# Optimization experiments

Hardware: AMD Instinct MI355X
Metric: run time of the kernel (lower is better)

Reference implementation:

```python
import jax, jax.numpy as jnp
import numpy as np

N_NODES = 100000
N_EDGES = 3200000
IN_DIM = 21
HID = 64


def gcn_conv(x, W, b, src, dst, n):
    # GCNConv: out = D^{-1/2} (A + I) D^{-1/2} (x W) + b
    h = x @ W  # [n, out]
    loop = jnp.arange(n)
    src_all = jnp.concatenate([src, loop])
    dst_all = jnp.concatenate([dst, loop])
    deg = jax.ops.segment_sum(jnp.ones(src_all.shape[0], h.dtype), dst_all,
                              num_segments=n)
    dinv = jax.lax.rsqrt(jnp.maximum(deg, 1.0))  # deg >= 1 with self-loops
    norm = dinv[src_all] * dinv[dst_all]  # [E+n]
    out = jax.ops.segment_sum(h[src_all] * norm[:, None], dst_all,
                              num_segments=n)
    return out + b


def setup_inputs() -> dict:
    key = jax.random.key(0)
    ks = jax.random.split(key, 12)
    def lin(k, fan_in, fan_out):
        bound = 1.0 / np.sqrt(fan_in)
        kw, kb = jax.random.split(k)
        W = jax.random.uniform(kw, (fan_in, fan_out), jnp.float32, -bound, bound)
        b = jax.random.uniform(kb, (fan_out,), jnp.float32, -bound, bound)
        return W, b
    x = jax.random.normal(ks[0], (N_NODES, IN_DIM), jnp.float32)
    edge_index = jax.random.randint(ks[1], (2, N_EDGES), 0, N_NODES, jnp.int64)
    W1, b1 = lin(ks[2], IN_DIM, HID)
    W2, b2 = lin(ks[3], HID, 2 * HID)
    W3, b3 = lin(ks[4], 2 * HID, HID)
    Wl1, bl1 = lin(ks[5], HID, 20)
    Wl2, bl2 = lin(ks[6], 20, 1)
    return {"x": x, "edge_index": edge_index,
            "W1": W1, "b1": b1, "W2": W2, "b2": b2, "W3": W3, "b3": b3,
            "Wl1": Wl1, "bl1": bl1, "Wl2": Wl2, "bl2": bl2}


def reference(x, edge_index, W1, b1, W2, b2, W3, b3, Wl1, bl1, Wl2, bl2):
    n = x.shape[0]
    src, dst = edge_index[0], edge_index[1]
    h = jax.nn.relu(gcn_conv(x, W1, b1, src, dst, n))
    h = jax.nn.relu(gcn_conv(h, W2, b2, src, dst, n))
    h = jax.nn.relu(gcn_conv(h, W3, b3, src, dst, n))
    h = jax.nn.relu(h @ Wl1 + bl1)
    return h @ Wl2 + bl2  # [n, 1]
```

## Files before the change

### kernel.cpp

```cpp
#include <hip/hip_runtime.h>

#define DEV static __device__ __forceinline__

typedef __attribute__((ext_vector_type(8))) short short8;
typedef __attribute__((ext_vector_type(4))) float f32x4;

DEV float bf2f(unsigned short u){ union{unsigned i; float f;} a; a.i=((unsigned)u)<<16; return a.f; }
DEV unsigned short f2bf(float f){ union{unsigned i; float f;} a; a.f=f; unsigned r=a.i+0x7fffu+((a.i>>16)&1u); return (unsigned short)(r>>16); }
DEV float2 bfu2f2(unsigned v){ union{unsigned i; float f;} lo,hi; lo.i=v<<16; hi.i=v&0xffff0000u; return make_float2(lo.f,hi.f); }

#define CB_SHIFT 9
#define CB_NODES 512
#define PK_SHIFT 23
#define PK_MASK  0x7fffffu
#define CHUNK 4096
#define P_WIN 4
#define BIN_CAP 18432

__global__ __launch_bounds__(256) void coarsehist_kernel(const int* __restrict__ dst,
    int* __restrict__ bcnt, int E, int NB){
  __shared__ int h[256];
  int t=threadIdx.x;
  h[t]=0; __syncthreads();
  int i=blockIdx.x*256+t, st=gridDim.x*256;
  for(;i<E;i+=st) atomicAdd(&h[dst[i]>>CB_SHIFT],1);
  __syncthreads();
  if(t<NB && h[t]) atomicAdd(&bcnt[t],h[t]);
}

__global__ __launch_bounds__(256) void binscan_kernel(const int* __restrict__ bcnt,
    int* __restrict__ binoffs, int* __restrict__ bincur, int NB, int E){
  __shared__ int s[256];
  int t=threadIdx.x;
  int v=(t<NB)?bcnt[t]:0;
  s[t]=v; __syncthreads();
  for(int o=1;o<256;o<<=1){
    int u=(t>=o)?s[t-o]:0;
    __syncthreads();
    if(t>=o) s[t]+=u;
    __syncthreads();
  }
  int ex=s[t]-v;
  if(t<NB){ binoffs[t]=ex; bincur[t]=ex; }
  if(t==0) binoffs[NB]=E;
}

__global__ __launch_bounds__(256) void chunkscatter_kernel(const int* __restrict__ src,
    const int* __restrict__ dst, int* __restrict__ bincur, unsigned* __restrict__ tmp,
    int E, int NB){
  __shared__ int lcnt[256];
  __shared__ int lstart[256];
  __shared__ int lbase[256];
  __shared__ unsigned pk[CHUNK];
  __shared__ int gaddr[CHUNK];
  int t=threadIdx.x;
  lcnt[t]=0; __syncthreads();
  int e0=blockIdx.x*CHUNK, e1=min(e0+CHUNK,E);
  int n=e1-e0;
  unsigned pkr[16]; int binr[16]; int rnk[16];
  #pragma unroll
  for(int q=0;q<16;q++){
    int i=e0+t+q*256;
    if(i<e1){
      int d=dst[i];
      int b=d>>CB_SHIFT;
      binr[q]=b;
      pkr[q]=(unsigned)src[i]|((unsigned)(d&(CB_NODES-1))<<PK_SHIFT);
      rnk[q]=atomicAdd(&lcnt[b],1);
    }
  }
  __syncthreads();
  int c=lcnt[t];
  lstart[t]=c; __syncthreads();
  for(int o=1;o<256;o<<=1){
    int u=(t>=o)?lstart[t-o]:0;
    __syncthreads();
    if(t>=o) lstart[t]+=u;
    __syncthreads();
  }
  int ex=lstart[t]-c;
  __syncthreads();
  lstart[t]=ex;
  lbase[t]=(t<NB&&c)?atomicAdd(&bincur[t],c):0;
  __syncthreads();
  #pragma unroll
  for(int q=0;q<16;q++){
    int i=e0+t+q*256;
    if(i<e1){
      int b=binr[q];
      int p=lstart[b]+rnk[q];
      pk[p]=pkr[q];
      gaddr[p]=lbase[b]+rnk[q];
    }
  }
  __syncthreads();
  for(int p=t;p<n;p+=256) tmp[gaddr[p]]=pk[p];
}

__global__ __launch_bounds__(512) void binsort_kernel(const unsigned* __restrict__ tmp,
    const int* __restrict__ binoffs, int* __restrict__ offs, int* __restrict__ deg,
    float* __restrict__ dinv, int* __restrict__ col, int M, int WSZ){
  __shared__ int cnt[CB_NODES*P_WIN];
  __shared__ int cur[CB_NODES*P_WIN];
  __shared__ int ssum[512];
  __shared__ int pkl[BIN_CAP];
  int b=blockIdx.x, t=threadIdx.x;
  int n0=b*CB_NODES;
  int e0=binoffs[b], e1=binoffs[b+1];
  int n=e1-e0;
  bool fit=(n<=BIN_CAP);
  cnt[4*t]=0; cnt[4*t+1]=0; cnt[4*t+2]=0; cnt[4*t+3]=0;
  __syncthreads();
  for(int i=e0+t;i<e1;i+=512){
    unsigned p=tmp[i];
    int s=(int)(p&PK_MASK);
    int w=(s>=WSZ)+(s>=2*WSZ)+(s>=3*WSZ);
    atomicAdd(&cnt[(int)(p>>PK_SHIFT)*P_WIN+w],1);
  }
  __syncthreads();
  int loc[4]; int s=0;
  #pragma unroll
  for(int q=0;q<4;q++){ loc[q]=s; s+=cnt[t*4+q]; }
  ssum[t]=s; __syncthreads();
  for(int o=1;o<512;o<<=1){
    int u=(t>=o)?ssum[t-o]:0;
    __syncthreads();
    if(t>=o) ssum[t]+=u;
    __syncthreads();
  }
  int rel=ssum[t]-s;
  #pragma unroll
  for(int q=0;q<4;q++) cur[t*4+q]=rel+loc[q];
  int nn=n0+t;
  if(nn<M){
    offs[nn]=e0+rel; deg[nn]=s; dinv[nn]=rsqrtf((float)(s+1));
  }
  __syncthreads();
  for(int i=e0+t;i<e1;i+=512){
    unsigned p=tmp[i];
    int s2=(int)(p&PK_MASK);
    int w=(s2>=WSZ)+(s2>=2*WSZ)+(s2>=3*WSZ);
    int pos=atomicAdd(&cur[(int)(p>>PK_SHIFT)*P_WIN+w],1);
    if(fit) pkl[pos]=s2;
    else col[e0+pos]=s2;
  }
  __syncthreads();
  if(fit){
    for(int i=t;i<n;i+=512) col[e0+i]=pkl[i];
  }
}

__global__ __launch_bounds__(256) void scale_kernel(const float* __restrict__ x, const float* __restrict__ dinv,
    uint2* __restrict__ xs, int M){
  int idx=blockIdx.x*256+threadIdx.x;
  if(idx>=M*8) return;
  int n=idx>>3, l=idx&7;
  float dv=dinv[n];
  const float* xr=x+(size_t)n*21;
  int c=4*l;
  float f0=(c  <21)?xr[c  ]*dv:0.f;
  float f1=(c+1<21)?xr[c+1]*dv:0.f;
  float f2v=(c+2<21)?xr[c+2]*dv:0.f;
  float f3=(c+3<21)?xr[c+3]*dv:0.f;
  uint2 v;
  v.x=(unsigned)f2bf(f0)|((unsigned)f2bf(f1)<<16);
  v.y=(unsigned)f2bf(f2v)|((unsigned)f2bf(f3)<<16);
  xs[(size_t)n*8+l]=v;
}

template<int GROUP,bool BR,bool OUTBF>
DEV void agg_body(const uint2* __restrict__ xs, const int* __restrict__ col,
    const int* __restrict__ offs, const int* __restrict__ deg, const float* __restrict__ dinv,
    const float* __restrict__ bias, void* __restrict__ out, int M){
  int gid=blockIdx.x*256+threadIdx.x;
  int node=gid/GROUP, lane=gid%GROUP;
  if(node>=M) return;
  float a0,a1,a2,a3;
  {
    uint2 v=xs[(size_t)node*GROUP+lane];
    float2 p=bfu2f2(v.x), q=bfu2f2(v.y);
    a0=p.x; a1=p.y; a2=q.x; a3=q.y;
  }
  int e0=offs[node], d=deg[node];
  int i=0;
  for(;i+8<=d;i+=8){
    int s[8]; uint2 w[8];
    #pragma unroll
    for(int q=0;q<8;q++) s[q]=col[e0+i+q];
    #pragma unroll
    for(int q=0;q<8;q++) w[q]=xs[(size_t)s[q]*GROUP+lane];
    #pragma unroll
    for(int q=0;q<8;q++){
      float2 p=bfu2f2(w[q].x); a0+=p.x; a1+=p.y;
      p=bfu2f2(w[q].y); a2+=p.x; a3+=p.y;
    }
  }
  for(;i+4<=d;i+=4){
    int s[4]; uint2 w[4];
    #pragma unroll
    for(int q=0;q<4;q++) s[q]=col[e0+i+q];
    #pragma unroll
    for(int q=0;q<4;q++) w[q]=xs[(size_t)s[q]*GROUP+lane];
    #pragma unroll
    for(int q=0;q<4;q++){
      float2 p=bfu2f2(w[q].x); a0+=p.x; a1+=p.y;
      p=bfu2f2(w[q].y); a2+=p.x; a3+=p.y;
    }
  }
  for(;i<d;i++){
    uint2 w=xs[(size_t)col[e0+i]*GROUP+lane];
    float2 p=bfu2f2(w.x); a0+=p.x; a1+=p.y;
    p=bfu2f2(w.y); a2+=p.x; a3+=p.y;
  }
  float dv=dinv[node];
  a0*=dv; a1*=dv; a2*=dv; a3*=dv;
  if constexpr(BR){
    a0=fmaxf(a0+bias[4*lane  ],0.f);
    a1=fmaxf(a1+bias[4*lane+1],0.f);
    a2=fmaxf(a2+bias[4*lane+2],0.f);
    a3=fmaxf(a3+bias[4*lane+3],0.f);
  }
  if constexpr(OUTBF){
    uint2 v;
    v.x=(unsigned)f2bf(a0)|((unsigned)f2bf(a1)<<16);
    v.y=(unsigned)f2bf(a2)|((unsigned)f2bf(a3)<<16);
    ((uint2*)out)[(size_t)node*GROUP+lane]=v;
  } else {
    ((float4*)out)[(size_t)node*GROUP+lane]=make_float4(a0,a1,a2,a3);
  }
}

__global__ __launch_bounds__(256) void agg1_kernel(const uint2* xs, const int* col, const int* offs,
    const int* deg, const float* dinv, uint2* out, int M){
  agg_body<8,false,true>(xs,col,offs,deg,dinv,nullptr,out,M);
}
__global__ __launch_bounds__(256) void agg2_kernel(const uint2* xs, const int* col, const int* offs,
    const int* deg, const float* dinv, uint2* out, int M){
  agg_body<16,false,true>(xs,col,offs,deg,dinv,nullptr,out,M);
}
__global__ __launch_bounds__(256) void agg3_kernel(const uint2* xs, const int* col, const int* offs,
    const int* deg, const float* dinv, const float* bias, float4* out, int M){
  agg_body<16,true,false>(xs,col,offs,deg,dinv,bias,out,M);
}

__global__ __launch_bounds__(256) void wprep_kernel(const float* __restrict__ W,
    unsigned short* __restrict__ Warr, int KS, int RK, int N, int KN){
  int idx=blockIdx.x*256+threadIdx.x;
  if(idx>=KN) return;
  int j=idx&7, l=(idx>>3)&63, t=idx>>9;
  int ks=t%KS, nt=t/KS;
  int k=ks*32+((l>>4)<<3)+j;
  int c=nt*16+(l&15);
  float w=(k<RK)?W[(size_t)k*N+c]:0.f;
  unsigned short hi=f2bf(w);
  unsigned short lo=f2bf(w-bf2f(hi));
  Warr[idx]=hi;
  Warr[KN+idx]=lo;
}

template<int K,int NT,bool BR,bool DV>
DEV void mfma_gemm_body(const unsigned short* __restrict__ X, const unsigned short* __restrict__ Warr,
    const float* __restrict__ bias, const float* __restrict__ dinv, unsigned short* __restrict__ Out, int M){
  constexpr int KS=K/32;
  constexpr int N=NT*16;
  constexpr int KN=K*N;
  int tid=threadIdx.x;
  int lane=tid&63, wave=tid>>6;
  int rowbase=blockIdx.x*64+wave*16;
  int r=rowbase+(lane&15);
  int rc=min(r,M-1);
  const short* Xr=(const short*)(X+(size_t)rc*K+((lane>>4)<<3));
  short8 af[KS];
  #pragma unroll
  for(int ks=0;ks<KS;ks++) af[ks]=*(const short8*)(Xr+ks*32);
  const short* wp=(const short*)Warr+lane*8;
  int colv=lane&15;
  #pragma unroll
  for(int nt=0;nt<NT;nt++){
    f32x4 acc={0.f,0.f,0.f,0.f};
    const short* wnt=wp+nt*KS*512;
    #pragma unroll
    for(int ks=0;ks<KS;ks++){
      short8 bh=*(const short8*)(wnt+ks*512);
      short8 bl=*(const short8*)(wnt+KN+ks*512);
      acc=__builtin_amdgcn_mfma_f32_16x16x32_bf16(af[ks],bh,acc,0,0,0);
      acc=__builtin_amdgcn_mfma_f32_16x16x32_bf16(af[ks],bl,acc,0,0,0);
    }
    int c=nt*16+colv;
    float bv=0.f;
    if constexpr(BR) bv=bias[c];
    #pragma unroll
    for(int reg=0;reg<4;reg++){
      int row=rowbase+((lane>>4)<<2)+reg;
      if(row<M){
        float v=acc[reg];
        if constexpr(BR) v=fmaxf(v+bv,0.f);
        if constexpr(DV) v*=dinv[row];
        Out[(size_t)row*N+c]=f2bf(v);
      }
    }
  }
}

__global__ __launch_bounds__(256) void gemm1m_kernel(const unsigned short* X, const unsigned short* Warr,
    const float* bias, const float* dinv, unsigned short* Out, int M){
  mfma_gemm_body<32,4,true,true>(X,Warr,bias,dinv,Out,M);
}
__global__ __launch_bounds__(256) void gemm2m_kernel(const unsigned short* X, const unsigned short* Warr,
    const float* bias, unsigned short* Out, int M){
  mfma_gemm_body<64,8,true,false>(X,Warr,bias,nullptr,Out,M);
}
__global__ __launch_bounds__(256) void gemm3m_kernel(const unsigned short* X, const unsigned short* Warr,
    const float* dinv, unsigned short* Out, int M){
  mfma_gemm_body<128,4,false,true>(X,Warr,nullptr,dinv,Out,M);
}

__global__ __launch_bounds__(256) void mlp_kernel(const float* __restrict__ h, const float* __restrict__ W1,
    const float* __restrict__ b1, const float* __restrict__ W2, const float* __restrict__ b2,
    float* __restrict__ out, int M){
  __shared__ float W1s[64*20];
  __shared__ float b1s[20];
  __shared__ float W2s[20];
  __shared__ float b2s;
  int tid=threadIdx.x;
  for(int i=tid;i<1280;i+=256) W1s[i]=W1[i];
  if(tid<20){ b1s[tid]=b1[tid]; W2s[tid]=W2[tid]; }
  if(tid==0) b2s=b2[0];
  __syncthreads();
  int n=blockIdx.x*256+tid;
  if(n>=M) return;
  float acc[20];
  #pragma unroll
  for(int j=0;j<20;j++) acc[j]=b1s[j];
  const float4* hp=(const float4*)(h+(size_t)n*64);
  for(int k4=0;k4<16;k4++){
    float4 hv=hp[k4];
    #pragma unroll
    for(int j=0;j<20;j++){
      acc[j]=fmaf(hv.x,W1s[(k4*4+0)*20+j],acc[j]);
      acc[j]=fmaf(hv.y,W1s[(k4*4+1)*20+j],acc[j]);
      acc[j]=fmaf(hv.z,W1s[(k4*4+2)*20+j],acc[j]);
      acc[j]=fmaf(hv.w,W1s[(k4*4+3)*20+j],acc[j]);
    }
  }
  float r=b2s;
  #pragma unroll
  for(int j=0;j<20;j++) r+=fmaxf(acc[j],0.f)*W2s[j];
  out[n]=r;
}

extern "C" void kernel_launch(void* const* d_in, const int* in_sizes, int n_in,
                              void* d_out, int out_size, void* d_ws, size_t ws_size,
                              hipStream_t stream){
  const float* x  =(const float*)d_in[0];
  const int*   ei =(const int*)  d_in[1];
  const float* W1 =(const float*)d_in[2];
  const float* b1 =(const float*)d_in[3];
  const float* W2 =(const float*)d_in[4];
  const float* b2 =(const float*)d_in[5];
  const float* W3 =(const float*)d_in[6];
  const float* b3 =(const float*)d_in[7];
  const float* Wl1=(const float*)d_in[8];
  const float* bl1=(const float*)d_in[9];
  const float* Wl2=(const float*)d_in[10];
  const float* bl2=(const float*)d_in[11];
  const int M=in_sizes[0]/21;
  const int E=in_sizes[1]/2;
  const int* srcp=ei;
  const int* dstp=ei+(size_t)E;
  const int NB=(M+CB_NODES-1)/CB_NODES;
  const int WSZ=(M+P_WIN-1)/P_WIN;

  char* ws=(char*)d_ws;
  size_t off=0;
  auto alloc=[&](size_t bytes)->void*{
    off=(off+255)&~(size_t)255;
    void* p=ws+off; off+=bytes; return p;
  };
  int*   offs   =(int*)  alloc((size_t)M*4);
  int*   deg    =(int*)  alloc((size_t)M*4);
  float* dinv   =(float*)alloc((size_t)M*4);
  int*   bcnt   =(int*)  alloc(256*4);
  int*   binoffs=(int*)  alloc(257*4);
  int*   bincur =(int*)  alloc(256*4);
  unsigned short* W1arr=(unsigned short*)alloc(2*32*64*2);
  unsigned short* W2arr=(unsigned short*)alloc(2*64*128*2);
  unsigned short* W3arr=(unsigned short*)alloc(2*128*64*2);
  int*   col    =(int*)  alloc((size_t)E*4);
  float* A=(float*)alloc((size_t)M*256);
  float* B=(float*)alloc((size_t)M*256);
  float* C=(float*)alloc((size_t)M*256);
  float* D=(float*)alloc((size_t)M*256);
  unsigned* tmp=(unsigned*)A;
  (void)ws_size;(void)n_in;(void)out_size;

  hipMemsetAsync(bcnt,0,256*4,stream);
  coarsehist_kernel<<<512,256,0,stream>>>(dstp,bcnt,E,NB);
  binscan_kernel<<<1,256,0,stream>>>(bcnt,binoffs,bincur,NB,E);
  chunkscatter_kernel<<<(E+CHUNK-1)/CHUNK,256,0,stream>>>(srcp,dstp,bincur,tmp,E,NB);
  binsort_kernel<<<NB,512,0,stream>>>(tmp,binoffs,offs,deg,dinv,col,M,WSZ);
  wprep_kernel<<<(32*64+255)/256,256,0,stream>>>(W1,W1arr,1,21,64,32*64);
  wprep_kernel<<<(64*128+255)/256,256,0,stream>>>(W2,W2arr,2,64,128,64*128);
  wprep_kernel<<<(128*64+255)/256,256,0,stream>>>(W3,W3arr,4,128,64,128*64);

  scale_kernel<<<(M*8+255)/256,256,0,stream>>>(x,dinv,(uint2*)A,M);
  agg1_kernel<<<(M*8+255)/256,256,0,stream>>>((const uint2*)A,col,offs,deg,dinv,(uint2*)B,M);
  gemm1m_kernel<<<(M+63)/64,256,0,stream>>>((const unsigned short*)B,W1arr,b1,dinv,(unsigned short*)C,M);
  agg2_kernel<<<(M*16+255)/256,256,0,stream>>>((const uint2*)C,col,offs,deg,dinv,(uint2*)D,M);
  gemm2m_kernel<<<(M+63)/64,256,0,stream>>>((const unsigned short*)D,W2arr,b2,(unsigned short*)A,M);
  gemm3m_kernel<<<(M+63)/64,256,0,stream>>>((const unsigned short*)A,W3arr,dinv,(unsigned short*)B,M);
  agg3_kernel<<<(M*16+255)/256,256,0,stream>>>((const uint2*)B,col,offs,deg,dinv,b3,(float4*)C,M);
  mlp_kernel<<<(M+255)/256,256,0,stream>>>(C,Wl1,bl1,Wl2,bl2,(float*)d_out,M);
}
```

Before: 284.0 us.

## Fuse layer-2/3 GEMMs via shared memory, bf16 agg3 output, unroll gather by 16

Merges the two back-to-back GEMMs (64->128 with bias+ReLU, then 128->64 with dinv scaling) into one kernel. The 128-wide intermediate stays in swizzled LDS instead of making a round trip through global memory. The final aggregation now writes bf16 instead of fp32, and the MLP reads bf16, which halves that traffic. The neighbour-gather loop is unrolled to 16 for more memory-level parallelism, at the cost of higher register pressure and extra bf16 rounding of the last hidden layer.

After: 276.9 us. 1.03x faster.

```diff
diff --git a/kernel.cpp b/kernel.cpp
--- a/kernel.cpp
+++ b/kernel.cpp
@@ -183,14 +183,14 @@
   }
   int e0=offs[node], d=deg[node];
   int i=0;
-  for(;i+8<=d;i+=8){
-    int s[8]; uint2 w[8];
-    #pragma unroll
-    for(int q=0;q<8;q++) s[q]=col[e0+i+q];
-    #pragma unroll
-    for(int q=0;q<8;q++) w[q]=xs[(size_t)s[q]*GROUP+lane];
-    #pragma unroll
-    for(int q=0;q<8;q++){
+  for(;i+16<=d;i+=16){
+    int s[16]; uint2 w[16];
+    #pragma unroll
+    for(int q=0;q<16;q++) s[q]=col[e0+i+q];
+    #pragma unroll
+    for(int q=0;q<16;q++) w[q]=xs[(size_t)s[q]*GROUP+lane];
+    #pragma unroll
+    for(int q=0;q<16;q++){
       float2 p=bfu2f2(w[q].x); a0+=p.x; a1+=p.y;
       p=bfu2f2(w[q].y); a2+=p.x; a3+=p.y;
     }
@@ -239,8 +239,8 @@
   agg_body<16,false,true>(xs,col,offs,deg,dinv,nullptr,out,M);
 }
 __global__ __launch_bounds__(256) void agg3_kernel(const uint2* xs, const int* col, const int* offs,
-    const int* deg, const float* dinv, const float* bias, float4* out, int M){
-  agg_body<16,true,false>(xs,col,offs,deg,dinv,bias,out,M);
+    const int* deg, const float* dinv, const float* bias, uint2* out, int M){
+  agg_body<16,true,true>(xs,col,offs,deg,dinv,bias,out,M);
 }
 
 __global__ __launch_bounds__(256) void wprep_kernel(const float* __restrict__ W,
@@ -306,16 +306,82 @@
     const float* bias, const float* dinv, unsigned short* Out, int M){
   mfma_gemm_body<32,4,true,true>(X,Warr,bias,dinv,Out,M);
 }
-__global__ __launch_bounds__(256) void gemm2m_kernel(const unsigned short* X, const unsigned short* Warr,
-    const float* bias, unsigned short* Out, int M){
-  mfma_gemm_body<64,8,true,false>(X,Warr,bias,nullptr,Out,M);
-}
-__global__ __launch_bounds__(256) void gemm3m_kernel(const unsigned short* X, const unsigned short* Warr,
-    const float* dinv, unsigned short* Out, int M){
-  mfma_gemm_body<128,4,false,true>(X,Warr,nullptr,dinv,Out,M);
-}
-
-__global__ __launch_bounds__(256) void mlp_kernel(const float* __restrict__ h, const float* __restrict__ W1,
+
+__global__ __launch_bounds__(256) void gemm23_kernel(const unsigned short* __restrict__ X,
+    const unsigned short* __restrict__ W2arr, const unsigned short* __restrict__ W3arr,
+    const float* __restrict__ bias2, const float* __restrict__ dinv,
+    unsigned short* __restrict__ Out, int M){
+  __shared__ unsigned short h2t[4*16*128];
+  int tid=threadIdx.x, lane=tid&63, wave=tid>>6;
+  int rowbase=blockIdx.x*64+wave*16;
+  unsigned short* base=h2t+wave*16*128;
+  {
+    int r=rowbase+(lane&15);
+    int rc=min(r,M-1);
+    const short* Xr=(const short*)(X+(size_t)rc*64+((lane>>4)<<3));
+    short8 af0=*(const short8*)(Xr);
+    short8 af1=*(const short8*)(Xr+32);
+    const short* wp=(const short*)W2arr+lane*8;
+    int colv=lane&15;
+    #pragma unroll
+    for(int nt=0;nt<8;nt++){
+      f32x4 acc={0.f,0.f,0.f,0.f};
+      const short* wnt=wp+nt*1024;
+      short8 bh0=*(const short8*)(wnt);
+      short8 bl0=*(const short8*)(wnt+8192);
+      short8 bh1=*(const short8*)(wnt+512);
+      short8 bl1=*(const short8*)(wnt+8704);
+      acc=__builtin_amdgcn_mfma_f32_16x16x32_bf16(af0,bh0,acc,0,0,0);
+      acc=__builtin_amdgcn_mfma_f32_16x16x32_bf16(af0,bl0,acc,0,0,0);
+      acc=__builtin_amdgcn_mfma_f32_16x16x32_bf16(af1,bh1,acc,0,0,0);
+      acc=__builtin_amdgcn_mfma_f32_16x16x32_bf16(af1,bl1,acc,0,0,0);
+      int c=nt*16+colv;
+      float bv=bias2[c];
+      #pragma unroll
+      for(int reg=0;reg<4;reg++){
+        int wr=((lane>>4)<<2)+reg;
+        float v=fmaxf(acc[reg]+bv,0.f);
+        int e=wr*128+(((((c>>3)^(wr&7)))<<3)|(c&7));
+        base[e]=f2bf(v);
+      }
+    }
+  }
+  __syncthreads();
+  {
+    int wr=lane&15;
+    short8 af[4];
+    #pragma unroll
+    for(int ks=0;ks<4;ks++){
+      int chunk=ks*4+(lane>>4);
+      int e=wr*128+((chunk^(wr&7))<<3);
+      af[ks]=*(const short8*)(base+e);
+    }
+    const short* wp=(const short*)W3arr+lane*8;
+    int colv=lane&15;
+    #pragma unroll
+    for(int nt=0;nt<4;nt++){
+      f32x4 acc={0.f,0.f,0.f,0.f};
+      const short* wnt=wp+nt*2048;
+      #pragma unroll
+      for(int ks=0;ks<4;ks++){
+        short8 bh=*(const short8*)(wnt+ks*512);
+        short8 bl=*(const short8*)(wnt+8192+ks*512);
+        acc=__builtin_amdgcn_mfma_f32_16x16x32_bf16(af[ks],bh,acc,0,0,0);
+        acc=__builtin_amdgcn_mfma_f32_16x16x32_bf16(af[ks],bl,acc,0,0,0);
+      }
+      int c=nt*16+colv;
+      #pragma unroll
+      for(int reg=0;reg<4;reg++){
+        int row=rowbase+((lane>>4)<<2)+reg;
+        if(row<M){
+          Out[(size_t)row*64+c]=f2bf(acc[reg]*dinv[row]);
+        }
+      }
+    }
+  }
+}
+
+__global__ __launch_bounds__(256) void mlp_kernel(const unsigned short* __restrict__ h, const float* __restrict__ W1,
     const float* __restrict__ b1, const float* __restrict__ W2, const float* __restrict__ b2,
     float* __restrict__ out, int M){
   __shared__ float W1s[64*20];
@@ -332,15 +398,16 @@
   float acc[20];
   #pragma unroll
   for(int j=0;j<20;j++) acc[j]=b1s[j];
-  const float4* hp=(const float4*)(h+(size_t)n*64);
+  const uint2* hp=(const uint2*)(h+(size_t)n*64);
   for(int k4=0;k4<16;k4++){
-    float4 hv=hp[k4];
+    uint2 v=hp[k4];
+    float2 p=bfu2f2(v.x), q=bfu2f2(v.y);
     #pragma unroll
     for(int j=0;j<20;j++){
-      acc[j]=fmaf(hv.x,W1s[(k4*4+0)*20+j],acc[j]);
-      acc[j]=fmaf(hv.y,W1s[(k4*4+1)*20+j],acc[j]);
-      acc[j]=fmaf(hv.z,W1s[(k4*4+2)*20+j],acc[j]);
-      acc[j]=fmaf(hv.w,W1s[(k4*4+3)*20+j],acc[j]);
+      acc[j]=fmaf(p.x,W1s[(k4*4+0)*20+j],acc[j]);
+      acc[j]=fmaf(p.y,W1s[(k4*4+1)*20+j],acc[j]);
+      acc[j]=fmaf(q.x,W1s[(k4*4+2)*20+j],acc[j]);
+      acc[j]=fmaf(q.y,W1s[(k4*4+3)*20+j],acc[j]);
     }
   }
   float r=b2s;
@@ -407,8 +474,7 @@
   agg1_kernel<<<(M*8+255)/256,256,0,stream>>>((const uint2*)A,col,offs,deg,dinv,(uint2*)B,M);
   gemm1m_kernel<<<(M+63)/64,256,0,stream>>>((const unsigned short*)B,W1arr,b1,dinv,(unsigned short*)C,M);
   agg2_kernel<<<(M*16+255)/256,256,0,stream>>>((const uint2*)C,col,offs,deg,dinv,(uint2*)D,M);
-  gemm2m_kernel<<<(M+63)/64,256,0,stream>>>((const unsigned short*)D,W2arr,b2,(unsigned short*)A,M);
-  gemm3m_kernel<<<(M+63)/64,256,0,stream>>>((const unsigned short*)A,W3arr,dinv,(unsigned short*)B,M);
-  agg3_kernel<<<(M*16+255)/256,256,0,stream>>>((const uint2*)B,col,offs,deg,dinv,b3,(float4*)C,M);
-  mlp_kernel<<<(M+255)/256,256,0,stream>>>(C,Wl1,bl1,Wl2,bl2,(float*)d_out,M);
-}
+  gemm23_kernel<<<(M+63)/64,256,0,stream>>>((const unsigned short*)D,W2arr,W3arr,b2,dinv,(unsigned short*)B,M);
+  agg3_kernel<<<(M*16+255)/256,256,0,stream>>>((const uint2*)B,col,offs,deg,dinv,b3,(uint2*)C,M);
+  mlp_kernel<<<(M+255)/256,256,0,stream>>>((const unsigned short*)C,Wl1,bl1,Wl2,bl2,(float*)d_out,M);
+}
```
